# Optimization experiments

Measured on AMD Instinct MI355X. Metric: run time of the kernel, lower is better.

## Reference

```python
import jax, jax.numpy as jnp
import numpy as np

N_T, N_C, N_I = 200000, 100000, 100000  # target / card / ip node counts
E = 300000                               # edges per relation
D, H, OUT = 128, 128, 2                  # embedding_size=in_size, hidden_size, out_size
# etype order: 0 card->target, 1 target->card, 2 ip->target, 3 target->ip


def setup_inputs() -> dict:
    key = jax.random.key(0)
    ks = jax.random.split(key, 14)
    return {
        "x_target": jax.random.normal(ks[0], (N_T, D), jnp.float32),
        "x_card": jax.random.normal(ks[1], (N_C, D), jnp.float32),
        "x_ip": jax.random.normal(ks[2], (N_I, D), jnp.float32),
        "w1": jax.random.normal(ks[3], (4, D, H), jnp.float32) / np.sqrt(D).astype(np.float32),
        "b1": jnp.zeros((4, H), jnp.float32),
        "w2": jax.random.normal(ks[4], (4, H, H), jnp.float32) / np.sqrt(H).astype(np.float32),
        "b2": jnp.zeros((4, H), jnp.float32),
        "w_out": jax.random.normal(ks[5], (H, OUT), jnp.float32) / np.sqrt(H).astype(np.float32),
        "b_out": jnp.zeros((OUT,), jnp.float32),
        "src0": jax.random.randint(ks[6], (E,), 0, N_C, jnp.int32),
        "dst0": jax.random.randint(ks[7], (E,), 0, N_T, jnp.int32),
        "src1": jax.random.randint(ks[8], (E,), 0, N_T, jnp.int32),
        "dst1": jax.random.randint(ks[9], (E,), 0, N_C, jnp.int32),
        "src2": jax.random.randint(ks[10], (E,), 0, N_I, jnp.int32),
        "dst2": jax.random.randint(ks[11], (E,), 0, N_T, jnp.int32),
        "src3": jax.random.randint(ks[12], (E,), 0, N_T, jnp.int32),
        "dst3": jax.random.randint(ks[13], (E,), 0, N_I, jnp.int32),
    }


def _mean_agg(msgs, dst, num_dst):
    # copy_u + mean reduce: segment-sum of gathered messages / in-degree (0 if no edges)
    s = jax.ops.segment_sum(msgs, dst, num_segments=num_dst)
    deg = jax.ops.segment_sum(jnp.ones((msgs.shape[0],), msgs.dtype), dst, num_segments=num_dst)
    return s / jnp.maximum(deg, 1.0)[:, None]


def _hetero_layer(feats, W, B, edges):
    # per-etype Linear on src feats, copy_u/mean per relation, sum across relations per dsttype
    out = {}
    for i, (src, dst, st, dt, nd) in enumerate(edges):
        Wh = feats[st] @ W[i] + B[i]          # [N_src, H] dense GEMM per etype
        agg = _mean_agg(Wh[src], dst, nd)      # gather + segment-mean (irregular)
        out[dt] = agg if dt not in out else out[dt] + agg
    return out


def reference(x_target, x_card, x_ip, w1, b1, w2, b2, w_out, b_out,
              src0, dst0, src1, dst1, src2, dst2, src3, dst3):
    edges = [
        (src0, dst0, "card", "target", N_T),
        (src1, dst1, "target", "card", N_C),
        (src2, dst2, "ip", "target", N_T),
        (src3, dst3, "target", "ip", N_I),
    ]
    h = {"target": x_target, "card": x_card, "ip": x_ip}
    h = _hetero_layer(h, w1, b1, edges)
    h = {k: jax.nn.leaky_relu(v) for k, v in h.items()}  # applied before layer i>0
    h = _hetero_layer(h, w2, b2, edges)
    logits = h["target"] @ w_out + b_out
    return jax.nn.softmax(logits, axis=-1)
```

## Files before the change

### kernel.cpp

```cpp
#include <hip/hip_runtime.h>


#define NT 200000
#define NCARD 100000
#define NIP 100000
#define NE 300000

typedef __attribute__((ext_vector_type(8))) short s8v;
typedef __attribute__((ext_vector_type(4))) float f4v;

__device__ __forceinline__ unsigned short f2b(float f) {
  unsigned u = __float_as_uint(f);
  u = (u + 0x7fff + ((u >> 16) & 1)) >> 16;
  return (unsigned short)u;
}


#define NB_HIST 4688
#define NB_WT 128
#define NB_CVT 25000

__global__ void front_k(const float* __restrict__ x, const float* __restrict__ w1,
                        const float* __restrict__ w2, const float* __restrict__ b2,
                        const float* __restrict__ wout,
                        const int* __restrict__ d1, const int* __restrict__ d3,
                        const int* __restrict__ d0, const int* __restrict__ d2,
                        int* __restrict__ deg1, int* __restrict__ deg3,
                        int* __restrict__ deg0, int* __restrict__ deg2,
                        int* __restrict__ rk1, int* __restrict__ rk3,
                        int* __restrict__ rk0, int* __restrict__ rk2,
                        unsigned short* __restrict__ xb, unsigned short* __restrict__ wtC,
                        unsigned short* __restrict__ wtI, float* __restrict__ wfC,
                        float* __restrict__ wfI, float* __restrict__ bfC,
                        float* __restrict__ bfI) {
  int bid = blockIdx.x, tid = threadIdx.x;
  if (bid < NB_HIST) {
    int t = bid * 256 + tid;
    if (t < NE) rk1[t] = atomicAdd(&deg1[d1[t]], 1);
    else if (t < 2 * NE) { int e = t - NE; rk3[e] = atomicAdd(&deg3[d3[e]], 1); }
    else if (t < 3 * NE) { int e = t - 2 * NE; rk0[e] = atomicAdd(&deg0[d0[e]], 1); }
    else if (t < 4 * NE) { int e = t - 3 * NE; rk2[e] = atomicAdd(&deg2[d2[e]], 1); }
  } else if (bid < NB_HIST + NB_WT) {
    int t = (bid - NB_HIST) * 256 + tid;
    int r = t >> 14;
    int n = (t >> 7) & 127, k = t & 127;
    const float* src = w1 + (r ? 3 : 1) * 16384;
    unsigned short* dst = r ? wtI : wtC;
    dst[n * 128 + k] = f2b(src[k * 128 + n]);
  } else if (bid == NB_HIST + NB_WT) {
    int k = tid >> 1, o = tid & 1;
    float sC = 0.f, sI = 0.f;
    for (int j = 0; j < 128; j++) {
      float wo = wout[j * 2 + o];
      sC += w2[0 * 16384 + k * 128 + j] * wo;
      sI += w2[2 * 16384 + k * 128 + j] * wo;
    }
    wfC[k * 2 + o] = sC;
    wfI[k * 2 + o] = sI;
    if (tid < 2) {
      float s = 0.f;
      for (int j = 0; j < 128; j++) s += b2[0 * 128 + j] * wout[j * 2 + tid];
      bfC[tid] = s;
    } else if (tid < 4) {
      int oo = tid - 2;
      float s = 0.f;
      for (int j = 0; j < 128; j++) s += b2[2 * 128 + j] * wout[j * 2 + oo];
      bfI[oo] = s;
    }
  } else {
    long i = (long)(bid - (NB_HIST + NB_WT + 1)) * 256 + tid;
    const long n4 = (long)NT * 128 / 4;
    if (i < n4) {
      float4 v = ((const float4*)x)[i];
      uint2 o;
      o.x = (unsigned)f2b(v.x) | ((unsigned)f2b(v.y) << 16);
      o.y = (unsigned)f2b(v.z) | ((unsigned)f2b(v.w) << 16);
      ((uint2*)xb)[i] = o;
    }
  }
}


__global__ void scan1q_k(const int* __restrict__ deg1, int* __restrict__ off1,
                         int* __restrict__ bs1, int nb1,
                         const int* __restrict__ deg3, int* __restrict__ off3,
                         int* __restrict__ bs3, int nb3,
                         const int* __restrict__ deg0, int* __restrict__ off0,
                         int* __restrict__ bs0, int nb0,
                         const int* __restrict__ deg2, int* __restrict__ off2,
                         int* __restrict__ bs2) {
  __shared__ int s[256];
  int bid = blockIdx.x;
  const int* deg; int* off; int* bsum; int N; int lb;
  if (bid < nb1) { deg = deg1; off = off1; bsum = bs1; N = NCARD; lb = bid; }
  else if (bid < nb1 + nb3) { deg = deg3; off = off3; bsum = bs3; N = NIP; lb = bid - nb1; }
  else if (bid < nb1 + nb3 + nb0) { deg = deg0; off = off0; bsum = bs0; N = NT; lb = bid - nb1 - nb3; }
  else { deg = deg2; off = off2; bsum = bs2; N = NT; lb = bid - nb1 - nb3 - nb0; }
  int tid = threadIdx.x;
  int i = lb * 256 + tid;
  int v = (i < N) ? deg[i] : 0;
  s[tid] = v;
  __syncthreads();
  for (int o = 1; o < 256; o <<= 1) {
    int t = (tid >= o) ? s[tid - o] : 0;
    __syncthreads();
    s[tid] += t;
    __syncthreads();
  }
  if (i < N) off[i] = s[tid] - v;
  if (tid == 255) bsum[lb] = s[255];
}

__global__ void scan2q_k(int* __restrict__ bs1, int nb1, int* __restrict__ bs3, int nb3,
                         int* __restrict__ bs0, int nb0, int* __restrict__ bs2, int nb2) {
  __shared__ int s[1024];
  int* bs; int nb;
  if (blockIdx.x == 0) { bs = bs1; nb = nb1; }
  else if (blockIdx.x == 1) { bs = bs3; nb = nb3; }
  else if (blockIdx.x == 2) { bs = bs0; nb = nb0; }
  else { bs = bs2; nb = nb2; }
  int t = threadIdx.x;
  int v = (t < nb) ? bs[t] : 0;
  s[t] = v;
  __syncthreads();
  for (int o = 1; o < 1024; o <<= 1) {
    int u = (t >= o) ? s[t - o] : 0;
    __syncthreads();
    s[t] += u;
    __syncthreads();
  }
  if (t < nb) bs[t] = s[t] - v;
}

__global__ void scan3q_k(int* __restrict__ off1, const int* __restrict__ bs1, int nb1,
                         int* __restrict__ off3, const int* __restrict__ bs3, int nb3,
                         int* __restrict__ off0, const int* __restrict__ bs0, int nb0,
                         int* __restrict__ off2, const int* __restrict__ bs2) {
  int bid = blockIdx.x;
  int* off; const int* bsum; int N; int lb;
  if (bid < nb1) { off = off1; bsum = bs1; N = NCARD; lb = bid; }
  else if (bid < nb1 + nb3) { off = off3; bsum = bs3; N = NIP; lb = bid - nb1; }
  else if (bid < nb1 + nb3 + nb0) { off = off0; bsum = bs0; N = NT; lb = bid - nb1 - nb3; }
  else { off = off2; bsum = bs2; N = NT; lb = bid - nb1 - nb3 - nb0; }
  int i = lb * 256 + threadIdx.x;
  if (i < N) off[i] += bsum[lb];
}


__global__ void fill4_k(const int* __restrict__ s1, const int* __restrict__ d1,
                        const int* __restrict__ rk1, const int* __restrict__ off1,
                        int* __restrict__ csr1,
                        const int* __restrict__ s3, const int* __restrict__ d3,
                        const int* __restrict__ rk3, const int* __restrict__ off3,
                        int* __restrict__ csr3,
                        const int* __restrict__ s0, const int* __restrict__ d0,
                        const int* __restrict__ rk0, const int* __restrict__ off0,
                        int* __restrict__ csr0,
                        const int* __restrict__ s2, const int* __restrict__ d2,
                        const int* __restrict__ rk2, const int* __restrict__ off2,
                        int* __restrict__ csr2) {
  int t = blockIdx.x * 256 + threadIdx.x;
  if (t < NE) csr1[off1[d1[t]] + rk1[t]] = s1[t];
  else if (t < 2 * NE) { int e = t - NE; csr3[off3[d3[e]] + rk3[e]] = s3[e]; }
  else if (t < 3 * NE) { int e = t - 2 * NE; csr0[off0[d0[e]] + rk0[e]] = s0[e]; }
  else if (t < 4 * NE) { int e = t - 3 * NE; csr2[off2[d2[e]] + rk2[e]] = s2[e]; }
}


__global__ void aggf_k(const unsigned short* __restrict__ xb,
                       const int* __restrict__ off1, const int* __restrict__ deg1,
                       const int* __restrict__ csr1, unsigned short* __restrict__ accC,
                       const int* __restrict__ off3, const int* __restrict__ deg3,
                       const int* __restrict__ csr3, unsigned short* __restrict__ accI) {
  int w = (blockIdx.x * 256 + threadIdx.x) >> 6;
  int lane = threadIdx.x & 63;
  if (w >= NCARD + NIP) return;
  const int* off; const int* deg; const int* csr; unsigned short* acc; int row;
  if (w < NCARD) { off = off1; deg = deg1; csr = csr1; acc = accC; row = w; }
  else { off = off3; deg = deg3; csr = csr3; acc = accI; row = w - NCARD; }
  int start = off[row], cnt = deg[row];
  int eg = lane >> 4, fl = lane & 15;
  float a[8] = {0.f, 0.f, 0.f, 0.f, 0.f, 0.f, 0.f, 0.f};
  for (int i = eg; i < cnt; i += 4) {
    int s = csr[start + i];
    uint4 v = *(const uint4*)(xb + (size_t)s * 128 + fl * 8);
    a[0] += __uint_as_float(v.x << 16);
    a[1] += __uint_as_float(v.x & 0xffff0000u);
    a[2] += __uint_as_float(v.y << 16);
    a[3] += __uint_as_float(v.y & 0xffff0000u);
    a[4] += __uint_as_float(v.z << 16);
    a[5] += __uint_as_float(v.z & 0xffff0000u);
    a[6] += __uint_as_float(v.w << 16);
    a[7] += __uint_as_float(v.w & 0xffff0000u);
  }
#pragma unroll
  for (int j = 0; j < 8; j++) {
    a[j] += __shfl_xor(a[j], 16);
    a[j] += __shfl_xor(a[j], 32);
  }
  if (eg == 0) {
    uint4 o;
    o.x = (unsigned)f2b(a[0]) | ((unsigned)f2b(a[1]) << 16);
    o.y = (unsigned)f2b(a[2]) | ((unsigned)f2b(a[3]) << 16);
    o.z = (unsigned)f2b(a[4]) | ((unsigned)f2b(a[5]) << 16);
    o.w = (unsigned)f2b(a[6]) | ((unsigned)f2b(a[7]) << 16);
    *(uint4*)(acc + (size_t)row * 128 + fl * 8) = o;
  }
}


__global__ __launch_bounds__(256) void gemm_mfma_k(
    const unsigned short* __restrict__ accC, const unsigned short* __restrict__ accI,
    const unsigned short* __restrict__ wtC, const unsigned short* __restrict__ wtI,
    const float* __restrict__ b1, const int* __restrict__ deg1,
    const int* __restrict__ deg3, const float* __restrict__ wfC,
    const float* __restrict__ wfI, const float* __restrict__ bfC,
    const float* __restrict__ bfI, float* __restrict__ zc, float* __restrict__ zi,
    int gbC) {
  int bid = blockIdx.x;
  const unsigned short* accb; const unsigned short* wt; const float* bias;
  const int* deg; const float* wf; const float* bf; float* zout; int M; int lb;
  if (bid < gbC) {
    accb = accC; wt = wtC; bias = b1 + 128; deg = deg1;
    wf = wfC; bf = bfC; zout = zc; M = NCARD; lb = bid;
  } else {
    accb = accI; wt = wtI; bias = b1 + 384; deg = deg3;
    wf = wfI; bf = bfI; zout = zi; M = NIP; lb = bid - gbC;
  }
  int wave = threadIdx.x >> 6, lane = threadIdx.x & 63;
  int q = lane >> 4, cl = lane & 15;
  int r0w = lb * 128 + wave * 32;

  s8v af[2][4];
#pragma unroll
  for (int rt = 0; rt < 2; rt++)
#pragma unroll
    for (int ks = 0; ks < 4; ks++)
      af[rt][ks] = *(const s8v*)(accb + (size_t)(r0w + rt * 16 + cl) * 128 + ks * 32 + q * 8);

  f4v acc[2][8];
#pragma unroll
  for (int rt = 0; rt < 2; rt++)
#pragma unroll
    for (int nt = 0; nt < 8; nt++) acc[rt][nt] = (f4v){0.f, 0.f, 0.f, 0.f};

#pragma unroll
  for (int nt = 0; nt < 8; nt++) {
#pragma unroll
    for (int ks = 0; ks < 4; ks++) {
      s8v bfr = *(const s8v*)(wt + (size_t)(nt * 16 + cl) * 128 + ks * 32 + q * 8);
      acc[0][nt] = __builtin_amdgcn_mfma_f32_16x16x32_bf16(af[0][ks], bfr, acc[0][nt], 0, 0, 0);
      acc[1][nt] = __builtin_amdgcn_mfma_f32_16x16x32_bf16(af[1][ks], bfr, acc[1][nt], 0, 0, 0);
    }
  }

  float2 wfv[8];
  float b1v[8];
#pragma unroll
  for (int nt = 0; nt < 8; nt++) {
    wfv[nt] = ((const float2*)wf)[nt * 16 + cl];
    b1v[nt] = bias[nt * 16 + cl];
  }
  float2 bf2 = *(const float2*)bf;
#pragma unroll
  for (int rt = 0; rt < 2; rt++) {
#pragma unroll
    for (int reg = 0; reg < 4; reg++) {
      int row = r0w + rt * 16 + q * 4 + reg;
      int d = (row < M) ? deg[row] : 0;
      float sc = (d > 0) ? 1.f / (float)d : 0.f;
      float p0 = 0.f, p1 = 0.f;
#pragma unroll
      for (int nt = 0; nt < 8; nt++) {
        float h = 0.f;
        if (d > 0) {
          h = acc[rt][nt][reg] * sc + b1v[nt];
          h = h > 0.f ? h : 0.01f * h;
        }
        p0 += h * wfv[nt].x;
        p1 += h * wfv[nt].y;
      }
#pragma unroll
      for (int o = 1; o < 16; o <<= 1) {
        p0 += __shfl_xor(p0, o);
        p1 += __shfl_xor(p1, o);
      }
      if (cl == 0 && row < M) {
        ((float2*)zout)[row] = make_float2(p0 + bf2.x, p1 + bf2.y);
      }
    }
  }
}


__global__ void finalg_k(const float* __restrict__ zc, const float* __restrict__ zi,
                         const int* __restrict__ off0, const int* __restrict__ deg0,
                         const int* __restrict__ csr0, const int* __restrict__ off2,
                         const int* __restrict__ deg2, const int* __restrict__ csr2,
                         const float* __restrict__ bout, float* __restrict__ out) {
  int t = blockIdx.x * 256 + threadIdx.x;
  if (t >= NT) return;
  float l0 = bout[0], l1 = bout[1];
  {
    int d = deg0[t], st = off0[t];
    if (d > 0) {
      float ax = 0.f, ay = 0.f;
      for (int i = 0; i < d; i++) {
        float2 z = ((const float2*)zc)[csr0[st + i]];
        ax += z.x; ay += z.y;
      }
      float inv = 1.f / (float)d;
      l0 += ax * inv; l1 += ay * inv;
    }
  }
  {
    int d = deg2[t], st = off2[t];
    if (d > 0) {
      float ax = 0.f, ay = 0.f;
      for (int i = 0; i < d; i++) {
        float2 z = ((const float2*)zi)[csr2[st + i]];
        ax += z.x; ay += z.y;
      }
      float inv = 1.f / (float)d;
      l0 += ax * inv; l1 += ay * inv;
    }
  }
  float m = fmaxf(l0, l1);
  float e0 = expf(l0 - m), e1 = expf(l1 - m);
  float inv = 1.f / (e0 + e1);
  ((float2*)out)[t] = make_float2(e0 * inv, e1 * inv);
}


extern "C" void kernel_launch(void* const* d_in, const int* in_sizes, int n_in,
                              void* d_out, int out_size, void* d_ws, size_t ws_size,
                              hipStream_t stream) {
  const float* x_target = (const float*)d_in[0];
  const float* w1 = (const float*)d_in[3];
  const float* b1 = (const float*)d_in[4];
  const float* w2 = (const float*)d_in[5];
  const float* b2 = (const float*)d_in[6];
  const float* wout = (const float*)d_in[7];
  const float* bout = (const float*)d_in[8];
  const int* src0 = (const int*)d_in[9];
  const int* dst0 = (const int*)d_in[10];
  const int* src1 = (const int*)d_in[11];
  const int* dst1 = (const int*)d_in[12];
  const int* src2 = (const int*)d_in[13];
  const int* dst2 = (const int*)d_in[14];
  const int* src3 = (const int*)d_in[15];
  const int* dst3 = (const int*)d_in[16];
  float* out = (float*)d_out;

  char* p = (char*)d_ws;
  auto alloc = [&](size_t bytes) -> char* {
    char* r = p;
    p += (bytes + 255) & ~(size_t)255;
    return r;
  };
  int* deg1 = (int*)alloc(NCARD * 4);
  int* deg3 = (int*)alloc(NIP * 4);
  int* deg0 = (int*)alloc(NT * 4);
  int* deg2 = (int*)alloc(NT * 4);
  size_t zero_bytes = (size_t)(p - (char*)d_ws);
  int* rk1 = (int*)alloc(NE * 4);
  int* rk3 = (int*)alloc(NE * 4);
  int* rk0 = (int*)alloc(NE * 4);
  int* rk2 = (int*)alloc(NE * 4);
  int* off1 = (int*)alloc(NCARD * 4);
  int* off3 = (int*)alloc(NIP * 4);
  int* off0 = (int*)alloc(NT * 4);
  int* off2 = (int*)alloc(NT * 4);
  int* bs1 = (int*)alloc(1024 * 4);
  int* bs3 = (int*)alloc(1024 * 4);
  int* bs0 = (int*)alloc(1024 * 4);
  int* bs2 = (int*)alloc(1024 * 4);
  int* csr1 = (int*)alloc(NE * 4);
  int* csr3 = (int*)alloc(NE * 4);
  int* csr0 = (int*)alloc(NE * 4);
  int* csr2 = (int*)alloc(NE * 4);
  unsigned short* xb = (unsigned short*)alloc((size_t)NT * 128 * 2);
  unsigned short* accC = (unsigned short*)alloc((size_t)NCARD * 128 * 2);
  unsigned short* accI = (unsigned short*)alloc((size_t)NIP * 128 * 2);
  alloc(128 * 128 * 2);
  unsigned short* wtC = (unsigned short*)alloc(16384 * 2);
  unsigned short* wtI = (unsigned short*)alloc(16384 * 2);
  float* zc = (float*)alloc((size_t)NCARD * 2 * 4);
  float* zi = (float*)alloc((size_t)NIP * 2 * 4);
  float* wfC = (float*)alloc(256 * 4);
  float* wfI = (float*)alloc(256 * 4);
  float* bfC = (float*)alloc(2 * 4);
  float* bfI = (float*)alloc(2 * 4);

  hipMemsetAsync(d_ws, 0, zero_bytes, stream);

  front_k<<<NB_HIST + NB_WT + 1 + NB_CVT, 256, 0, stream>>>(
      x_target, w1, w2, b2, wout, dst1, dst3, dst0, dst2, deg1, deg3, deg0, deg2,
      rk1, rk3, rk0, rk2, xb, wtC, wtI, wfC, wfI, bfC, bfI);

  int nb1 = (NCARD + 255) / 256, nb3 = (NIP + 255) / 256;
  int nb0 = (NT + 255) / 256, nb2 = (NT + 255) / 256;
  scan1q_k<<<nb1 + nb3 + nb0 + nb2, 256, 0, stream>>>(
      deg1, off1, bs1, nb1, deg3, off3, bs3, nb3, deg0, off0, bs0, nb0, deg2, off2, bs2);
  scan2q_k<<<4, 1024, 0, stream>>>(bs1, nb1, bs3, nb3, bs0, nb0, bs2, nb2);
  scan3q_k<<<nb1 + nb3 + nb0 + nb2, 256, 0, stream>>>(
      off1, bs1, nb1, off3, bs3, nb3, off0, bs0, nb0, off2, bs2);

  fill4_k<<<(4 * NE + 255) / 256, 256, 0, stream>>>(
      src1, dst1, rk1, off1, csr1, src3, dst3, rk3, off3, csr3,
      src0, dst0, rk0, off0, csr0, src2, dst2, rk2, off2, csr2);

  aggf_k<<<(NCARD + NIP + 3) / 4, 256, 0, stream>>>(xb, off1, deg1, csr1, accC,
                                                    off3, deg3, csr3, accI);

  int gbC = (NCARD + 127) / 128, gbI = (NIP + 127) / 128;
  gemm_mfma_k<<<gbC + gbI, 256, 0, stream>>>(accC, accI, wtC, wtI, b1, deg1, deg3,
                                             wfC, wfI, bfC, bfI, zc, zi, gbC);

  finalg_k<<<(NT + 255) / 256, 256, 0, stream>>>(zc, zi, off0, deg0, csr0,
                                                 off2, deg2, csr2, bout, out);
}
```

Before: 409.0 us.

## Replace global atomic degree histogram with chunked LDS histograms and drop memset

Degree counting moves from global atomics per edge to blocks that each own a range of destination nodes and an edge chunk. Each block builds its histogram in shared memory, then writes per-chunk counts to scratch that aliases the accC buffer. The scan kernel turns the per-chunk counts into chunk-local prefixes plus a total degree, and the fill kernel adds the chunk prefix when placing edges, so the memset of the degree arrays is no longer needed. The bf16 conversion also now handles two float4 per thread. In exchange, every edge list is re-read by many range blocks, and there is extra per-chunk scratch traffic.

Result: slower. 431.8 us (+5.6%).

```diff
diff --git a/kernel.cpp b/kernel.cpp
--- a/kernel.cpp
+++ b/kernel.cpp
@@ -6,6 +6,15 @@
 #define NIP 100000
 #define NE 300000
 
+#define RANGE 8192
+#define NCHUNK 8
+#define CHUNK 37500
+#define RB1 13
+#define RB3 13
+#define RB0 25
+#define RB2 25
+#define NB_HISTA ((RB1 + RB3 + RB0 + RB2) * NCHUNK)
+
 typedef __attribute__((ext_vector_type(8))) short s8v;
 typedef __attribute__((ext_vector_type(4))) float f4v;
 
@@ -16,17 +25,16 @@
 }
 
 
-#define NB_HIST 4688
 #define NB_WT 128
-#define NB_CVT 25000
+#define NB_CVT 12500
 
 __global__ void front_k(const float* __restrict__ x, const float* __restrict__ w1,
                         const float* __restrict__ w2, const float* __restrict__ b2,
                         const float* __restrict__ wout,
                         const int* __restrict__ d1, const int* __restrict__ d3,
                         const int* __restrict__ d0, const int* __restrict__ d2,
-                        int* __restrict__ deg1, int* __restrict__ deg3,
-                        int* __restrict__ deg0, int* __restrict__ deg2,
+                        int* __restrict__ h1, int* __restrict__ h3,
+                        int* __restrict__ h0, int* __restrict__ h2,
                         int* __restrict__ rk1, int* __restrict__ rk3,
                         int* __restrict__ rk0, int* __restrict__ rk2,
                         unsigned short* __restrict__ xb, unsigned short* __restrict__ wtC,
@@ -34,20 +42,34 @@
                         float* __restrict__ wfI, float* __restrict__ bfC,
                         float* __restrict__ bfI) {
   int bid = blockIdx.x, tid = threadIdx.x;
-  if (bid < NB_HIST) {
-    int t = bid * 256 + tid;
-    if (t < NE) rk1[t] = atomicAdd(&deg1[d1[t]], 1);
-    else if (t < 2 * NE) { int e = t - NE; rk3[e] = atomicAdd(&deg3[d3[e]], 1); }
-    else if (t < 3 * NE) { int e = t - 2 * NE; rk0[e] = atomicAdd(&deg0[d0[e]], 1); }
-    else if (t < 4 * NE) { int e = t - 3 * NE; rk2[e] = atomicAdd(&deg2[d2[e]], 1); }
-  } else if (bid < NB_HIST + NB_WT) {
-    int t = (bid - NB_HIST) * 256 + tid;
+  if (bid < NB_HISTA) {
+    __shared__ int hsh[RANGE];
+    int rb = bid >> 3, c = bid & 7;
+    const int* d; int* hist; int* rkl; int N; int lo;
+    if (rb < RB1) { d = d1; hist = h1; rkl = rk1; N = NCARD; lo = rb * RANGE; }
+    else if (rb < RB1 + RB3) { d = d3; hist = h3; rkl = rk3; N = NIP; lo = (rb - RB1) * RANGE; }
+    else if (rb < RB1 + RB3 + RB0) { d = d0; hist = h0; rkl = rk0; N = NT; lo = (rb - RB1 - RB3) * RANGE; }
+    else { d = d2; hist = h2; rkl = rk2; N = NT; lo = (rb - RB1 - RB3 - RB0) * RANGE; }
+    for (int b = tid; b < RANGE; b += 256) hsh[b] = 0;
+    __syncthreads();
+    int e1 = (c + 1) * CHUNK;
+    for (int e = c * CHUNK + tid; e < e1; e += 256) {
+      int key = d[e] - lo;
+      if ((unsigned)key < (unsigned)RANGE) rkl[e] = atomicAdd(&hsh[key], 1);
+    }
+    __syncthreads();
+    for (int b = tid; b < RANGE; b += 256) {
+      int g = lo + b;
+      if (g < N) hist[(size_t)c * N + g] = hsh[b];
+    }
+  } else if (bid < NB_HISTA + NB_WT) {
+    int t = (bid - NB_HISTA) * 256 + tid;
     int r = t >> 14;
     int n = (t >> 7) & 127, k = t & 127;
     const float* src = w1 + (r ? 3 : 1) * 16384;
     unsigned short* dst = r ? wtI : wtC;
     dst[n * 128 + k] = f2b(src[k * 128 + n]);
-  } else if (bid == NB_HIST + NB_WT) {
+  } else if (bid == NB_HISTA + NB_WT) {
     int k = tid >> 1, o = tid & 1;
     float sC = 0.f, sI = 0.f;
     for (int j = 0; j < 128; j++) {
@@ -68,37 +90,51 @@
       bfI[oo] = s;
     }
   } else {
-    long i = (long)(bid - (NB_HIST + NB_WT + 1)) * 256 + tid;
-    const long n4 = (long)NT * 128 / 4;
-    if (i < n4) {
-      float4 v = ((const float4*)x)[i];
-      uint2 o;
-      o.x = (unsigned)f2b(v.x) | ((unsigned)f2b(v.y) << 16);
-      o.y = (unsigned)f2b(v.z) | ((unsigned)f2b(v.w) << 16);
-      ((uint2*)xb)[i] = o;
-    }
-  }
-}
-
-
-__global__ void scan1q_k(const int* __restrict__ deg1, int* __restrict__ off1,
-                         int* __restrict__ bs1, int nb1,
-                         const int* __restrict__ deg3, int* __restrict__ off3,
-                         int* __restrict__ bs3, int nb3,
-                         const int* __restrict__ deg0, int* __restrict__ off0,
-                         int* __restrict__ bs0, int nb0,
-                         const int* __restrict__ deg2, int* __restrict__ off2,
-                         int* __restrict__ bs2) {
+    long i = (long)(bid - (NB_HISTA + NB_WT + 1)) * 512 + tid;
+    const float4* x4 = (const float4*)x;
+    float4 va = x4[i];
+    float4 vb = x4[i + 256];
+    uint2 oa, ob;
+    oa.x = (unsigned)f2b(va.x) | ((unsigned)f2b(va.y) << 16);
+    oa.y = (unsigned)f2b(va.z) | ((unsigned)f2b(va.w) << 16);
+    ob.x = (unsigned)f2b(vb.x) | ((unsigned)f2b(vb.y) << 16);
+    ob.y = (unsigned)f2b(vb.z) | ((unsigned)f2b(vb.w) << 16);
+    ((uint2*)xb)[i] = oa;
+    ((uint2*)xb)[i + 256] = ob;
+  }
+}
+
+
+__global__ void scan1q_k(int* __restrict__ h1, int* __restrict__ deg1,
+                         int* __restrict__ off1, int* __restrict__ bs1, int nb1,
+                         int* __restrict__ h3, int* __restrict__ deg3,
+                         int* __restrict__ off3, int* __restrict__ bs3, int nb3,
+                         int* __restrict__ h0, int* __restrict__ deg0,
+                         int* __restrict__ off0, int* __restrict__ bs0, int nb0,
+                         int* __restrict__ h2, int* __restrict__ deg2,
+                         int* __restrict__ off2, int* __restrict__ bs2) {
   __shared__ int s[256];
   int bid = blockIdx.x;
-  const int* deg; int* off; int* bsum; int N; int lb;
-  if (bid < nb1) { deg = deg1; off = off1; bsum = bs1; N = NCARD; lb = bid; }
-  else if (bid < nb1 + nb3) { deg = deg3; off = off3; bsum = bs3; N = NIP; lb = bid - nb1; }
-  else if (bid < nb1 + nb3 + nb0) { deg = deg0; off = off0; bsum = bs0; N = NT; lb = bid - nb1 - nb3; }
-  else { deg = deg2; off = off2; bsum = bs2; N = NT; lb = bid - nb1 - nb3 - nb0; }
+  int* hist; int* deg; int* off; int* bsum; int N; int lb;
+  if (bid < nb1) { hist = h1; deg = deg1; off = off1; bsum = bs1; N = NCARD; lb = bid; }
+  else if (bid < nb1 + nb3) { hist = h3; deg = deg3; off = off3; bsum = bs3; N = NIP; lb = bid - nb1; }
+  else if (bid < nb1 + nb3 + nb0) { hist = h0; deg = deg0; off = off0; bsum = bs0; N = NT; lb = bid - nb1 - nb3; }
+  else { hist = h2; deg = deg2; off = off2; bsum = bs2; N = NT; lb = bid - nb1 - nb3 - nb0; }
   int tid = threadIdx.x;
   int i = lb * 256 + tid;
-  int v = (i < N) ? deg[i] : 0;
+  int v = 0;
+  if (i < N) {
+    int acc = 0;
+#pragma unroll
+    for (int c = 0; c < NCHUNK; c++) {
+      size_t idx = (size_t)c * N + i;
+      int t = hist[idx];
+      hist[idx] = acc;
+      acc += t;
+    }
+    deg[i] = acc;
+    v = acc;
+  }
   s[tid] = v;
   __syncthreads();
   for (int o = 1; o < 256; o <<= 1) {
@@ -149,21 +185,30 @@
 
 __global__ void fill4_k(const int* __restrict__ s1, const int* __restrict__ d1,
                         const int* __restrict__ rk1, const int* __restrict__ off1,
-                        int* __restrict__ csr1,
+                        const int* __restrict__ h1, int* __restrict__ csr1,
                         const int* __restrict__ s3, const int* __restrict__ d3,
                         const int* __restrict__ rk3, const int* __restrict__ off3,
-                        int* __restrict__ csr3,
+                        const int* __restrict__ h3, int* __restrict__ csr3,
                         const int* __restrict__ s0, const int* __restrict__ d0,
                         const int* __restrict__ rk0, const int* __restrict__ off0,
-                        int* __restrict__ csr0,
+                        const int* __restrict__ h0, int* __restrict__ csr0,
                         const int* __restrict__ s2, const int* __restrict__ d2,
                         const int* __restrict__ rk2, const int* __restrict__ off2,
-                        int* __restrict__ csr2) {
+                        const int* __restrict__ h2, int* __restrict__ csr2) {
   int t = blockIdx.x * 256 + threadIdx.x;
-  if (t < NE) csr1[off1[d1[t]] + rk1[t]] = s1[t];
-  else if (t < 2 * NE) { int e = t - NE; csr3[off3[d3[e]] + rk3[e]] = s3[e]; }
-  else if (t < 3 * NE) { int e = t - 2 * NE; csr0[off0[d0[e]] + rk0[e]] = s0[e]; }
-  else if (t < 4 * NE) { int e = t - 3 * NE; csr2[off2[d2[e]] + rk2[e]] = s2[e]; }
+  if (t < NE) {
+    int e = t, c = e / CHUNK, dd = d1[e];
+    csr1[off1[dd] + h1[(size_t)c * NCARD + dd] + rk1[e]] = s1[e];
+  } else if (t < 2 * NE) {
+    int e = t - NE, c = e / CHUNK, dd = d3[e];
+    csr3[off3[dd] + h3[(size_t)c * NIP + dd] + rk3[e]] = s3[e];
+  } else if (t < 3 * NE) {
+    int e = t - 2 * NE, c = e / CHUNK, dd = d0[e];
+    csr0[off0[dd] + h0[(size_t)c * NT + dd] + rk0[e]] = s0[e];
+  } else if (t < 4 * NE) {
+    int e = t - 3 * NE, c = e / CHUNK, dd = d2[e];
+    csr2[off2[dd] + h2[(size_t)c * NT + dd] + rk2[e]] = s2[e];
+  }
 }
 
 
@@ -362,7 +407,6 @@
   int* deg3 = (int*)alloc(NIP * 4);
   int* deg0 = (int*)alloc(NT * 4);
   int* deg2 = (int*)alloc(NT * 4);
-  size_t zero_bytes = (size_t)(p - (char*)d_ws);
   int* rk1 = (int*)alloc(NE * 4);
   int* rk3 = (int*)alloc(NE * 4);
   int* rk0 = (int*)alloc(NE * 4);
@@ -392,23 +436,27 @@
   float* bfC = (float*)alloc(2 * 4);
   float* bfI = (float*)alloc(2 * 4);
 
-  hipMemsetAsync(d_ws, 0, zero_bytes, stream);
-
-  front_k<<<NB_HIST + NB_WT + 1 + NB_CVT, 256, 0, stream>>>(
-      x_target, w1, w2, b2, wout, dst1, dst3, dst0, dst2, deg1, deg3, deg0, deg2,
+  int* h1 = (int*)accC;
+  int* h3 = h1 + (size_t)NCHUNK * NCARD;
+  int* h0 = h3 + (size_t)NCHUNK * NIP;
+  int* h2 = h0 + (size_t)NCHUNK * NT;
+
+  front_k<<<NB_HISTA + NB_WT + 1 + NB_CVT, 256, 0, stream>>>(
+      x_target, w1, w2, b2, wout, dst1, dst3, dst0, dst2, h1, h3, h0, h2,
       rk1, rk3, rk0, rk2, xb, wtC, wtI, wfC, wfI, bfC, bfI);
 
   int nb1 = (NCARD + 255) / 256, nb3 = (NIP + 255) / 256;
   int nb0 = (NT + 255) / 256, nb2 = (NT + 255) / 256;
   scan1q_k<<<nb1 + nb3 + nb0 + nb2, 256, 0, stream>>>(
-      deg1, off1, bs1, nb1, deg3, off3, bs3, nb3, deg0, off0, bs0, nb0, deg2, off2, bs2);
+      h1, deg1, off1, bs1, nb1, h3, deg3, off3, bs3, nb3,
+      h0, deg0, off0, bs0, nb0, h2, deg2, off2, bs2);
   scan2q_k<<<4, 1024, 0, stream>>>(bs1, nb1, bs3, nb3, bs0, nb0, bs2, nb2);
   scan3q_k<<<nb1 + nb3 + nb0 + nb2, 256, 0, stream>>>(
       off1, bs1, nb1, off3, bs3, nb3, off0, bs0, nb0, off2, bs2);
 
   fill4_k<<<(4 * NE + 255) / 256, 256, 0, stream>>>(
-      src1, dst1, rk1, off1, csr1, src3, dst3, rk3, off3, csr3,
-      src0, dst0, rk0, off0, csr0, src2, dst2, rk2, off2, csr2);
+      src1, dst1, rk1, off1, h1, csr1, src3, dst3, rk3, off3, h3, csr3,
+      src0, dst0, rk0, off0, h0, csr0, src2, dst2, rk2, off2, h2, csr2);
 
   aggf_k<<<(NCARD + NIP + 3) / 4, 256, 0, stream>>>(xb, off1, deg1, csr1, accC,
                                                     off3, deg3, csr3, accI);
```
